# Kernel optimization log

Measured on AMD Instinct MI355X. Metric: run time of the kernel, lower is better.

The kernel has to match this reference:

```python
import jax, jax.numpy as jnp
import numpy as np

V, E, H, L, B, S = 32000, 512, 1024, 2, 128, 256

def setup_inputs() -> dict:
    key = jax.random.key(0)
    ks = jax.random.split(key, 24)
    s = 0.02
    inp = {
        'input_token': jax.random.randint(ks[0], (B, 1), 0, V),
        'hidden': jax.random.normal(ks[1], (L, B, H), jnp.float32),
        'cell': jax.random.normal(ks[2], (L, B, H), jnp.float32),
        'encoder_outputs': jax.random.normal(ks[3], (B, S, H), jnp.float32),
        'embedding': jax.random.normal(ks[4], (V, E), jnp.float32) * s,
        'W1_w': jax.random.normal(ks[5], (H, H), jnp.float32) * s,
        'W1_b': jnp.zeros((H,), jnp.float32),
        'W2_w': jax.random.normal(ks[6], (H, H), jnp.float32) * s,
        'W2_b': jnp.zeros((H,), jnp.float32),
        'V_w': jax.random.normal(ks[7], (1, H), jnp.float32) * s,
        'V_b': jnp.zeros((1,), jnp.float32),
        'w_ih0': jax.random.normal(ks[8], (4 * H, E + H), jnp.float32) * s,
        'w_hh0': jax.random.normal(ks[9], (4 * H, H), jnp.float32) * s,
        'b_ih0': jnp.zeros((4 * H,), jnp.float32),
        'b_hh0': jnp.zeros((4 * H,), jnp.float32),
        'w_ih1': jax.random.normal(ks[10], (4 * H, H), jnp.float32) * s,
        'w_hh1': jax.random.normal(ks[11], (4 * H, H), jnp.float32) * s,
        'b_ih1': jnp.zeros((4 * H,), jnp.float32),
        'b_hh1': jnp.zeros((4 * H,), jnp.float32),
        'fc_w': jax.random.normal(ks[12], (V, 2 * H), jnp.float32) * s,
        'fc_b': jnp.zeros((V,), jnp.float32),
    }
    return inp


def _lstm_cell(x, h, c, w_ih, w_hh, b_ih, b_hh):
    # PyTorch gate order: i, f, g, o
    gates = x @ w_ih.T + b_ih + h @ w_hh.T + b_hh  # [B, 4H]
    i, f, g, o = jnp.split(gates, 4, axis=-1)
    i, f, o = jax.nn.sigmoid(i), jax.nn.sigmoid(f), jax.nn.sigmoid(o)
    g = jnp.tanh(g)
    c_new = f * c + i * g
    h_new = o * jnp.tanh(c_new)
    return h_new, c_new


def reference(input_token, hidden, cell, encoder_outputs, embedding,
              W1_w, W1_b, W2_w, W2_b, V_w, V_b,
              w_ih0, w_hh0, b_ih0, b_hh0, w_ih1, w_hh1, b_ih1, b_hh1,
              fc_w, fc_b):
    emb = embedding[input_token[:, 0]]                       # [B, E]
    h_top = hidden[-1]                                        # [B, H]
    # Bahdanau attention
    energy = jnp.tanh(encoder_outputs @ W1_w.T + W1_b
                      + (h_top @ W2_w.T + W2_b)[:, None, :])  # [B, S, H]
    scores = energy @ V_w.T + V_b                             # [B, S, 1]
    attn = jax.nn.softmax(scores, axis=1)                     # [B, S, 1]
    context = jnp.sum(attn * encoder_outputs, axis=1)         # [B, H]
    # single-step 2-layer LSTM
    x = jnp.concatenate([emb, context], axis=-1)              # [B, E+H]
    h0, c0 = _lstm_cell(x, hidden[0], cell[0], w_ih0, w_hh0, b_ih0, b_hh0)
    h1, c1 = _lstm_cell(h0, hidden[1], cell[1], w_ih1, w_hh1, b_ih1, b_hh1)
    # output projection
    logits = jnp.concatenate([h1, context], axis=-1) @ fc_w.T + fc_b  # [B, V]
    prediction = jax.nn.log_softmax(logits, axis=-1)
    new_hidden = jnp.stack([h0, h1])
    new_cell = jnp.stack([c0, c1])
    return prediction, new_hidden, new_cell, attn
```

## Files before the change

### kernel.cpp

```cpp
#include <hip/hip_runtime.h>

#define H_DIM 1024
#define B_DIM 128
#define S_DIM 256
#define V_DIM 32000
#define E_DIM 512

typedef __bf16 bf16_t;
typedef bf16_t bf16x8 __attribute__((ext_vector_type(8)));
typedef bf16_t bf16x4 __attribute__((ext_vector_type(4)));
typedef float floatx4 __attribute__((ext_vector_type(4)));

#define BM 128
#define BN 128
#define BK 64
#define LDK (BK + 8)

__device__ inline float fast_tanh(float x) {
    x = fminf(fmaxf(x, -15.f), 15.f);
    float e = __expf(2.f * x);
    return (e - 1.f) / (e + 1.f);
}
__device__ inline float sigmoidf_(float x) { return 1.f / (1.f + __expf(-x)); }

__device__ inline bf16x4 cvt4(float4 v) {
    return (bf16x4){(bf16_t)v.x, (bf16_t)v.y, (bf16_t)v.z, (bf16_t)v.w};
}

template <int MODE>
__global__ __launch_bounds__(256) void gemm2(
    const float* __restrict__ A, int lda,
    const float* __restrict__ B1, int ldb1,
    const float* __restrict__ B2, int ldb2, int splitB,
    int K, int kChunk,
    float* __restrict__ C, int ldc,
    const float* __restrict__ bias1, const float* __restrict__ bias2,
    const float* __restrict__ proj, const float* __restrict__ Vw,
    float* __restrict__ scores)
{
    __shared__ bf16_t As[BM][LDK];
    __shared__ bf16_t Bs[BN][LDK];

    const int tid  = threadIdx.x;
    const int wid  = tid >> 6;
    const int lane = tid & 63;
    const int m0 = blockIdx.y * BM;
    const int n0 = blockIdx.x * BN;

    const int wave_m = (wid & 1) * 64;
    const int wave_n = (wid >> 1) * 64;
    const int laneM  = lane & 15;
    const int laneK  = (lane >> 4) * 8;

    const int tk = (tid & 15) * 4;
    const int tr = tid >> 4;

    const int kStart = blockIdx.z * kChunk;
    const int kEnd   = min(K, kStart + kChunk);

    floatx4 acc[4][4];
#pragma unroll
    for (int i = 0; i < 4; i++)
#pragma unroll
        for (int j = 0; j < 4; j++) acc[i][j] = (floatx4)0.f;

    const float* Arow = A + (size_t)(m0 + tr) * lda + tk;

    for (int k0 = kStart; k0 < kEnd; k0 += BK) {
#pragma unroll
        for (int p = 0; p < 8; p++) {
            float4 v = *(const float4*)(Arow + (size_t)(p * 16) * lda + k0);
            *(bf16x4*)(&As[tr + p * 16][tk]) = cvt4(v);
        }
        const float* Bp; size_t ldb; int kb;
        if (k0 < splitB) { Bp = B1; ldb = (size_t)ldb1; kb = k0 + tk; }
        else             { Bp = B2; ldb = (size_t)ldb2; kb = k0 - splitB + tk; }
        const float* Brow = Bp + (size_t)(n0 + tr) * ldb + kb;
#pragma unroll
        for (int p = 0; p < 8; p++) {
            float4 v = *(const float4*)(Brow + (size_t)(p * 16) * ldb);
            *(bf16x4*)(&Bs[tr + p * 16][tk]) = cvt4(v);
        }
        __syncthreads();

#pragma unroll
        for (int kk = 0; kk < 2; kk++) {
            bf16x8 af[4], bfb[4];
#pragma unroll
            for (int mt = 0; mt < 4; mt++)
                af[mt] = *(const bf16x8*)(&As[wave_m + mt * 16 + laneM][kk * 32 + laneK]);
#pragma unroll
            for (int nt = 0; nt < 4; nt++)
                bfb[nt] = *(const bf16x8*)(&Bs[wave_n + nt * 16 + laneM][kk * 32 + laneK]);
#pragma unroll
            for (int mt = 0; mt < 4; mt++)
#pragma unroll
                for (int nt = 0; nt < 4; nt++)
                    acc[mt][nt] = __builtin_amdgcn_mfma_f32_16x16x32_bf16(
                        af[mt], bfb[nt], acc[mt][nt], 0, 0, 0);
        }
        __syncthreads();
    }

    if (MODE == 0 || MODE == 2) {
        const bool addb = (MODE == 0) || (blockIdx.z == 0);
#pragma unroll
        for (int mt = 0; mt < 4; mt++) {
            int mrow = m0 + wave_m + mt * 16 + (lane >> 4) * 4;
#pragma unroll
            for (int nt = 0; nt < 4; nt++) {
                int n = n0 + wave_n + nt * 16 + laneM;
                float bsum = 0.f;
                if (addb) bsum = (bias1 ? bias1[n] : 0.f) + (bias2 ? bias2[n] : 0.f);
#pragma unroll
                for (int r = 0; r < 4; r++) {
                    float val = acc[mt][nt][r] + bsum;
                    if (MODE == 0) C[(size_t)(mrow + r) * ldc + n] = val;
                    else           atomicAdd(&C[(size_t)(mrow + r) * ldc + n], val);
                }
            }
        }
    } else {
#pragma unroll
        for (int mt = 0; mt < 4; mt++) {
#pragma unroll
            for (int r = 0; r < 4; r++) {
                int m = m0 + wave_m + mt * 16 + (lane >> 4) * 4 + r;
                int b = m >> 8;
                float v = 0.f;
#pragma unroll
                for (int nt = 0; nt < 4; nt++) {
                    int n = n0 + wave_n + nt * 16 + laneM;
                    float t = acc[mt][nt][r] + bias1[n] + proj[(size_t)b * H_DIM + n];
                    v += fast_tanh(t) * Vw[n];
                }
#pragma unroll
                for (int off = 1; off < 16; off <<= 1) v += __shfl_xor(v, off, 64);
                if (laneM == 0) atomicAdd(&scores[m], v);
            }
        }
    }
}

__global__ void attn_softmax_kernel(const float* __restrict__ scores,
                                    float* __restrict__ attn_ws,
                                    float* __restrict__ attn_out) {
    __shared__ float red[256];
    int b = blockIdx.x, t = threadIdx.x;
    float v = scores[b * S_DIM + t];
    red[t] = v; __syncthreads();
    for (int off = 128; off > 0; off >>= 1) {
        if (t < off) red[t] = fmaxf(red[t], red[t + off]);
        __syncthreads();
    }
    float mx = red[0]; __syncthreads();
    float e = __expf(v - mx);
    red[t] = e; __syncthreads();
    for (int off = 128; off > 0; off >>= 1) {
        if (t < off) red[t] += red[t + off];
        __syncthreads();
    }
    float a = e / red[0];
    attn_ws[b * S_DIM + t] = a;
    attn_out[b * S_DIM + t] = a;
}

__global__ __launch_bounds__(256) void context_kernel(
    const float* __restrict__ enc, const float* __restrict__ attn,
    float* __restrict__ x0, float* __restrict__ x2) {
    __shared__ float a_s[S_DIM];
    int b = blockIdx.y;
    int h = blockIdx.x * 256 + threadIdx.x;
    a_s[threadIdx.x] = attn[b * S_DIM + threadIdx.x];
    __syncthreads();
    const float* base = enc + (size_t)b * S_DIM * H_DIM + h;
    float acc0 = 0.f, acc1 = 0.f;
#pragma unroll 4
    for (int s = 0; s < S_DIM; s += 2) {
        acc0 += a_s[s]     * base[(size_t)s * H_DIM];
        acc1 += a_s[s + 1] * base[(size_t)(s + 1) * H_DIM];
    }
    float c = acc0 + acc1;
    x0[(size_t)b * 2560 + 512 + h]  = c;
    x2[(size_t)b * 2048 + 1024 + h] = c;
}

__global__ void pack_misc_kernel(const int* __restrict__ tok,
                                 const float* __restrict__ emb_table,
                                 const float* __restrict__ hidden,
                                 float* __restrict__ x0, float* __restrict__ x1) {
    int b = blockIdx.y;
    int k = blockIdx.x * 256 + threadIdx.x;
    if (k < E_DIM)
        x0[(size_t)b * 2560 + k] = emb_table[(size_t)tok[b] * E_DIM + k];
    else if (k < E_DIM + H_DIM)
        x0[(size_t)b * 2560 + 1024 + k] = hidden[b * H_DIM + (k - E_DIM)];
    else
        x1[(size_t)b * 2048 + 1024 + (k - E_DIM - H_DIM)] =
            hidden[(size_t)B_DIM * H_DIM + b * H_DIM + (k - E_DIM - H_DIM)];
}

__global__ void lstm_cell_kernel(const float* __restrict__ gates,
                                 const float* __restrict__ c_in,
                                 float* __restrict__ hx, int hx_stride,
                                 float* __restrict__ h_out,
                                 float* __restrict__ c_out) {
    int b = blockIdx.y;
    int n = blockIdx.x * 256 + threadIdx.x;
    const float* g = gates + (size_t)b * 4 * H_DIM;
    float i  = sigmoidf_(g[n]);
    float f  = sigmoidf_(g[H_DIM + n]);
    float gg = fast_tanh(g[2 * H_DIM + n]);
    float o  = sigmoidf_(g[3 * H_DIM + n]);
    float c  = f * c_in[b * H_DIM + n] + i * gg;
    float h  = o * fast_tanh(c);
    hx[(size_t)b * hx_stride + n] = h;
    h_out[b * H_DIM + n] = h;
    c_out[b * H_DIM + n] = c;
}

__global__ __launch_bounds__(1024) void log_softmax_kernel(float* logits) {
    __shared__ float red[1024];
    int b = blockIdx.x, t = threadIdx.x;
    float* row = logits + (size_t)b * V_DIM;
    float mx = -1e30f;
    for (int v = t; v < V_DIM; v += 1024) mx = fmaxf(mx, row[v]);
    red[t] = mx; __syncthreads();
    for (int off = 512; off > 0; off >>= 1) {
        if (t < off) red[t] = fmaxf(red[t], red[t + off]);
        __syncthreads();
    }
    mx = red[0]; __syncthreads();
    float s = 0.f;
    for (int v = t; v < V_DIM; v += 1024) s += __expf(row[v] - mx);
    red[t] = s; __syncthreads();
    for (int off = 512; off > 0; off >>= 1) {
        if (t < off) red[t] += red[t + off];
        __syncthreads();
    }
    float lse = mx + __logf(red[0]);
    for (int v = t; v < V_DIM; v += 1024) row[v] = row[v] - lse;
}

extern "C" void kernel_launch(void* const* d_in, const int* in_sizes, int n_in,
                              void* d_out, int out_size, void* d_ws, size_t ws_size,
                              hipStream_t stream) {
    const int*   tok    = (const int*)  d_in[0];
    const float* hidden = (const float*)d_in[1];
    const float* cell   = (const float*)d_in[2];
    const float* enc    = (const float*)d_in[3];
    const float* embt   = (const float*)d_in[4];
    const float* W1w    = (const float*)d_in[5];
    const float* W1b    = (const float*)d_in[6];
    const float* W2w    = (const float*)d_in[7];
    const float* W2b    = (const float*)d_in[8];
    const float* Vw     = (const float*)d_in[9];
    const float* wih0 = (const float*)d_in[11];
    const float* whh0 = (const float*)d_in[12];
    const float* bih0 = (const float*)d_in[13];
    const float* bhh0 = (const float*)d_in[14];
    const float* wih1 = (const float*)d_in[15];
    const float* whh1 = (const float*)d_in[16];
    const float* bih1 = (const float*)d_in[17];
    const float* bhh1 = (const float*)d_in[18];
    const float* fcw  = (const float*)d_in[19];
    const float* fcb  = (const float*)d_in[20];

    float* out        = (float*)d_out;
    float* pred       = out;
    float* out_hidden = out + (size_t)B_DIM * V_DIM;
    float* out_cell   = out_hidden + 2 * B_DIM * H_DIM;
    float* out_attn   = out_cell + 2 * B_DIM * H_DIM;

    float* ws     = (float*)d_ws;
    float* scores = ws;
    float* proj   = scores + 32768;
    float* gatesA = proj + 131072;
    float* gatesB = gatesA + 524288;
    float* attnw  = gatesB + 524288;
    float* x0     = attnw + 32768;
    float* x1     = x0 + 327680;
    float* x2     = x1 + 262144;

    hipMemsetAsync(ws, 0, (size_t)(32768 + 131072 + 2 * 524288) * sizeof(float), stream);

    dim3 blk(256);
    pack_misc_kernel<<<dim3(10, B_DIM), blk, 0, stream>>>(tok, embt, hidden, x0, x1);

    gemm2<2><<<dim3(8, 1, 2), blk, 0, stream>>>(
        hidden + (size_t)B_DIM * H_DIM, H_DIM, W2w, H_DIM, nullptr, 0, H_DIM,
        H_DIM, 512, proj, H_DIM, W2b, nullptr, nullptr, nullptr, nullptr);

    gemm2<1><<<dim3(8, 256, 1), blk, 0, stream>>>(
        enc, H_DIM, W1w, H_DIM, nullptr, 0, H_DIM,
        H_DIM, H_DIM, nullptr, 0, W1b, nullptr, proj, Vw, scores);

    attn_softmax_kernel<<<B_DIM, 256, 0, stream>>>(scores, attnw, out_attn);
    context_kernel<<<dim3(4, B_DIM), blk, 0, stream>>>(enc, attnw, x0, x2);

    gemm2<2><<<dim3(32, 1, 4), blk, 0, stream>>>(
        x0, 2560, wih0, 1536, whh0, H_DIM, 1536,
        2560, 640, gatesA, 4096, bih0, bhh0, nullptr, nullptr, nullptr);
    lstm_cell_kernel<<<dim3(4, B_DIM), blk, 0, stream>>>(
        gatesA, cell, x1, 2048, out_hidden, out_cell);

    gemm2<2><<<dim3(32, 1, 4), blk, 0, stream>>>(
        x1, 2048, wih1, H_DIM, whh1, H_DIM, H_DIM,
        2048, 512, gatesB, 4096, bih1, bhh1, nullptr, nullptr, nullptr);
    lstm_cell_kernel<<<dim3(4, B_DIM), blk, 0, stream>>>(
        gatesB, cell + (size_t)B_DIM * H_DIM, x2, 2048,
        out_hidden + (size_t)B_DIM * H_DIM, out_cell + (size_t)B_DIM * H_DIM);

    gemm2<0><<<dim3(250, 1, 1), blk, 0, stream>>>(
        x2, 2048, fcw, 2048, nullptr, 0, 2048,
        2048, 2048, pred, V_DIM, fcb, nullptr, nullptr, nullptr, nullptr);

    log_softmax_kernel<<<B_DIM, 1024, 0, stream>>>(pred);
}
```

Baseline: 813.1 us.

## Overhaul decoder kernels: bf16 scores GEMM, prefetch, split-K partials, fused softmax-context

Adds register prefetch of the next K tile in the generic GEMM, fuses attention softmax with the context reduction, and replaces atomic split-K with separate partial buffers that the LSTM cell and log-softmax kernels sum. When the workspace is large enough, it converts encoder outputs and W1 to bf16 and runs a dedicated scores GEMM that loads straight into LDS with a swizzled layout. The FC projection is split over K to raise occupancy. The cost is extra conversion passes over the 32 MB encoder tensor on every call, more workspace traffic for the partials, and paths chosen by workspace size.

```diff
diff --git a/kernel.cpp b/kernel.cpp
--- a/kernel.cpp
+++ b/kernel.cpp
@@ -22,9 +22,103 @@
     return (e - 1.f) / (e + 1.f);
 }
 __device__ inline float sigmoidf_(float x) { return 1.f / (1.f + __expf(-x)); }
-
 __device__ inline bf16x4 cvt4(float4 v) {
     return (bf16x4){(bf16_t)v.x, (bf16_t)v.y, (bf16_t)v.z, (bf16_t)v.w};
+}
+__device__ __forceinline__ void gload16(const bf16_t* g, bf16_t* l) {
+    __builtin_amdgcn_global_load_lds(
+        (const __attribute__((address_space(1))) void*)g,
+        (__attribute__((address_space(3))) void*)l, 16, 0, 0);
+}
+
+__global__ __launch_bounds__(256) void gemm_scores_bf16(
+    const bf16_t* __restrict__ A, const bf16_t* __restrict__ B,
+    const float* __restrict__ bias1, const float* __restrict__ proj,
+    const float* __restrict__ Vw, float* __restrict__ scores)
+{
+    __shared__ bf16_t As[128 * 64];
+    __shared__ bf16_t Bs[128 * 64];
+
+    const int tid  = threadIdx.x;
+    const int wid  = tid >> 6;
+    const int lane = tid & 63;
+    const int m0 = blockIdx.y * BM;
+    const int n0 = blockIdx.x * BN;
+
+    const int wave_m = (wid & 1) * 64;
+    const int wave_n = (wid >> 1) * 64;
+    const int laneM  = lane & 15;
+    const int laneG  = lane >> 4;
+
+    const int srow = lane >> 3;
+    const int pc   = lane & 7;
+
+    floatx4 acc[4][4];
+#pragma unroll
+    for (int i = 0; i < 4; i++)
+#pragma unroll
+        for (int j = 0; j < 4; j++) acc[i][j] = (floatx4)0.f;
+
+    for (int k0 = 0; k0 < H_DIM; k0 += BK) {
+#pragma unroll
+        for (int i = 0; i < 4; i++) {
+            int r  = wid * 32 + i * 8 + srow;
+            int lc = pc ^ (r & 7);
+            gload16(A + (size_t)(m0 + r) * H_DIM + k0 + lc * 8,
+                    As + (wid * 32 + i * 8) * 64);
+        }
+#pragma unroll
+        for (int i = 0; i < 4; i++) {
+            int r  = wid * 32 + i * 8 + srow;
+            int lc = pc ^ (r & 7);
+            gload16(B + (size_t)(n0 + r) * H_DIM + k0 + lc * 8,
+                    Bs + (wid * 32 + i * 8) * 64);
+        }
+        __syncthreads();
+
+#pragma unroll
+        for (int kk = 0; kk < 2; kk++) {
+            bf16x8 af[4], bfb[4];
+#pragma unroll
+            for (int mt = 0; mt < 4; mt++) {
+                int ra = wave_m + mt * 16 + laneM;
+                int pa = (kk * 4 + laneG) ^ (ra & 7);
+                af[mt] = *(const bf16x8*)(&As[ra * 64 + pa * 8]);
+            }
+#pragma unroll
+            for (int nt = 0; nt < 4; nt++) {
+                int rb = wave_n + nt * 16 + laneM;
+                int pb = (kk * 4 + laneG) ^ (rb & 7);
+                bfb[nt] = *(const bf16x8*)(&Bs[rb * 64 + pb * 8]);
+            }
+#pragma unroll
+            for (int mt = 0; mt < 4; mt++)
+#pragma unroll
+                for (int nt = 0; nt < 4; nt++)
+                    acc[mt][nt] = __builtin_amdgcn_mfma_f32_16x16x32_bf16(
+                        af[mt], bfb[nt], acc[mt][nt], 0, 0, 0);
+        }
+        __syncthreads();
+    }
+
+#pragma unroll
+    for (int mt = 0; mt < 4; mt++) {
+#pragma unroll
+        for (int r = 0; r < 4; r++) {
+            int m = m0 + wave_m + mt * 16 + (lane >> 4) * 4 + r;
+            int b = m >> 8;
+            float v = 0.f;
+#pragma unroll
+            for (int nt = 0; nt < 4; nt++) {
+                int n = n0 + wave_n + nt * 16 + laneM;
+                float t = acc[mt][nt][r] + bias1[n] + proj[(size_t)b * H_DIM + n];
+                v += fast_tanh(t) * Vw[n];
+            }
+#pragma unroll
+            for (int off = 1; off < 16; off <<= 1) v += __shfl_xor(v, off, 64);
+            if (laneM == 0) atomicAdd(&scores[m], v);
+        }
+    }
 }
 
 template <int MODE>
@@ -34,6 +128,7 @@
     const float* __restrict__ B2, int ldb2, int splitB,
     int K, int kChunk,
     float* __restrict__ C, int ldc,
+    float* __restrict__ Cpart, long long partStride,
     const float* __restrict__ bias1, const float* __restrict__ bias2,
     const float* __restrict__ proj, const float* __restrict__ Vw,
     float* __restrict__ scores)
@@ -66,23 +161,31 @@
 
     const float* Arow = A + (size_t)(m0 + tr) * lda + tk;
 
-    for (int k0 = kStart; k0 < kEnd; k0 += BK) {
-#pragma unroll
-        for (int p = 0; p < 8; p++) {
-            float4 v = *(const float4*)(Arow + (size_t)(p * 16) * lda + k0);
-            *(bf16x4*)(&As[tr + p * 16][tk]) = cvt4(v);
-        }
+    float4 ar[8], br[8];
+    auto loadA = [&](int k0) {
+#pragma unroll
+        for (int p = 0; p < 8; p++)
+            ar[p] = *(const float4*)(Arow + (size_t)(p * 16) * lda + k0);
+    };
+    auto loadB = [&](int k0) {
         const float* Bp; size_t ldb; int kb;
         if (k0 < splitB) { Bp = B1; ldb = (size_t)ldb1; kb = k0 + tk; }
         else             { Bp = B2; ldb = (size_t)ldb2; kb = k0 - splitB + tk; }
         const float* Brow = Bp + (size_t)(n0 + tr) * ldb + kb;
 #pragma unroll
-        for (int p = 0; p < 8; p++) {
-            float4 v = *(const float4*)(Brow + (size_t)(p * 16) * ldb);
-            *(bf16x4*)(&Bs[tr + p * 16][tk]) = cvt4(v);
-        }
-        __syncthreads();
-
+        for (int p = 0; p < 8; p++)
+            br[p] = *(const float4*)(Brow + (size_t)(p * 16) * ldb);
+    };
+
+    loadA(kStart); loadB(kStart);
+
+    for (int k0 = kStart; k0 < kEnd; k0 += BK) {
+#pragma unroll
+        for (int p = 0; p < 8; p++) *(bf16x4*)(&As[tr + p * 16][tk]) = cvt4(ar[p]);
+#pragma unroll
+        for (int p = 0; p < 8; p++) *(bf16x4*)(&Bs[tr + p * 16][tk]) = cvt4(br[p]);
+        __syncthreads();
+        if (k0 + BK < kEnd) { loadA(k0 + BK); loadB(k0 + BK); }
 #pragma unroll
         for (int kk = 0; kk < 2; kk++) {
             bf16x8 af[4], bfb[4];
@@ -102,8 +205,11 @@
         __syncthreads();
     }
 
-    if (MODE == 0 || MODE == 2) {
-        const bool addb = (MODE == 0) || (blockIdx.z == 0);
+    if (MODE == 2 || MODE == 3) {
+        const bool addb = (blockIdx.z == 0);
+        float* dst = C;
+        if (MODE == 3 && blockIdx.z > 0)
+            dst = Cpart + (size_t)(blockIdx.z - 1) * partStride;
 #pragma unroll
         for (int mt = 0; mt < 4; mt++) {
             int mrow = m0 + wave_m + mt * 16 + (lane >> 4) * 4;
@@ -115,8 +221,8 @@
 #pragma unroll
                 for (int r = 0; r < 4; r++) {
                     float val = acc[mt][nt][r] + bsum;
-                    if (MODE == 0) C[(size_t)(mrow + r) * ldc + n] = val;
-                    else           atomicAdd(&C[(size_t)(mrow + r) * ldc + n], val);
+                    if (MODE == 2) atomicAdd(&C[(size_t)(mrow + r) * ldc + n], val);
+                    else           dst[(size_t)(mrow + r) * ldc + n] = val;
                 }
             }
         }
@@ -142,10 +248,23 @@
     }
 }
 
-__global__ void attn_softmax_kernel(const float* __restrict__ scores,
-                                    float* __restrict__ attn_ws,
-                                    float* __restrict__ attn_out) {
+__global__ void convert_kernel(const float* __restrict__ src,
+                               bf16_t* __restrict__ dst, int n4) {
+    int i = blockIdx.x * blockDim.x + threadIdx.x;
+    int stride = gridDim.x * blockDim.x;
+    for (; i < n4; i += stride) {
+        float4 v = ((const float4*)src)[i];
+        ((bf16x4*)dst)[i] = cvt4(v);
+    }
+}
+
+template <typename T>
+__global__ __launch_bounds__(256) void softmax_context_kernel(
+    const T* __restrict__ enc, const float* __restrict__ scores,
+    float* __restrict__ out_attn, float* __restrict__ x0, float* __restrict__ x2)
+{
     __shared__ float red[256];
+    __shared__ float a_s[256];
     int b = blockIdx.x, t = threadIdx.x;
     float v = scores[b * S_DIM + t];
     red[t] = v; __syncthreads();
@@ -161,28 +280,29 @@
         __syncthreads();
     }
     float a = e / red[0];
-    attn_ws[b * S_DIM + t] = a;
-    attn_out[b * S_DIM + t] = a;
-}
-
-__global__ __launch_bounds__(256) void context_kernel(
-    const float* __restrict__ enc, const float* __restrict__ attn,
-    float* __restrict__ x0, float* __restrict__ x2) {
-    __shared__ float a_s[S_DIM];
-    int b = blockIdx.y;
-    int h = blockIdx.x * 256 + threadIdx.x;
-    a_s[threadIdx.x] = attn[b * S_DIM + threadIdx.x];
+    out_attn[b * S_DIM + t] = a;
+    a_s[t] = a;
     __syncthreads();
-    const float* base = enc + (size_t)b * S_DIM * H_DIM + h;
-    float acc0 = 0.f, acc1 = 0.f;
+
+    const T* base = enc + (size_t)b * S_DIM * H_DIM;
+    float c0 = 0.f, c1 = 0.f, c2 = 0.f, c3 = 0.f;
 #pragma unroll 4
-    for (int s = 0; s < S_DIM; s += 2) {
-        acc0 += a_s[s]     * base[(size_t)s * H_DIM];
-        acc1 += a_s[s + 1] * base[(size_t)(s + 1) * H_DIM];
-    }
-    float c = acc0 + acc1;
-    x0[(size_t)b * 2560 + 512 + h]  = c;
-    x2[(size_t)b * 2048 + 1024 + h] = c;
+    for (int s = 0; s < S_DIM; s++) {
+        float aw = a_s[s];
+        const T* row = base + (size_t)s * H_DIM + t;
+        c0 += aw * (float)row[0];
+        c1 += aw * (float)row[256];
+        c2 += aw * (float)row[512];
+        c3 += aw * (float)row[768];
+    }
+    x0[(size_t)b * 2560 + 512 + t]        = c0;
+    x0[(size_t)b * 2560 + 512 + t + 256]  = c1;
+    x0[(size_t)b * 2560 + 512 + t + 512]  = c2;
+    x0[(size_t)b * 2560 + 512 + t + 768]  = c3;
+    x2[(size_t)b * 2048 + 1024 + t]       = c0;
+    x2[(size_t)b * 2048 + 1024 + t + 256] = c1;
+    x2[(size_t)b * 2048 + 1024 + t + 512] = c2;
+    x2[(size_t)b * 2048 + 1024 + t + 768] = c3;
 }
 
 __global__ void pack_misc_kernel(const int* __restrict__ tok,
@@ -201,30 +321,52 @@
 }
 
 __global__ void lstm_cell_kernel(const float* __restrict__ gates,
+                                 const float* __restrict__ gpart, int nExtra,
+                                 long long partStride,
                                  const float* __restrict__ c_in,
                                  float* __restrict__ hx, int hx_stride,
                                  float* __restrict__ h_out,
                                  float* __restrict__ c_out) {
     int b = blockIdx.y;
     int n = blockIdx.x * 256 + threadIdx.x;
-    const float* g = gates + (size_t)b * 4 * H_DIM;
-    float i  = sigmoidf_(g[n]);
-    float f  = sigmoidf_(g[H_DIM + n]);
-    float gg = fast_tanh(g[2 * H_DIM + n]);
-    float o  = sigmoidf_(g[3 * H_DIM + n]);
-    float c  = f * c_in[b * H_DIM + n] + i * gg;
-    float h  = o * fast_tanh(c);
+    size_t base = (size_t)b * 4 * H_DIM;
+    float gi = gates[base + n];
+    float gf = gates[base + H_DIM + n];
+    float gg = gates[base + 2 * H_DIM + n];
+    float go = gates[base + 3 * H_DIM + n];
+    for (int p = 0; p < nExtra; p++) {
+        size_t pb = (size_t)p * partStride + base;
+        gi += gpart[pb + n];
+        gf += gpart[pb + H_DIM + n];
+        gg += gpart[pb + 2 * H_DIM + n];
+        go += gpart[pb + 3 * H_DIM + n];
+    }
+    float i = sigmoidf_(gi), f = sigmoidf_(gf), o = sigmoidf_(go);
+    float g = fast_tanh(gg);
+    float c = f * c_in[b * H_DIM + n] + i * g;
+    float h = o * fast_tanh(c);
     hx[(size_t)b * hx_stride + n] = h;
     h_out[b * H_DIM + n] = h;
     c_out[b * H_DIM + n] = c;
 }
 
-__global__ __launch_bounds__(1024) void log_softmax_kernel(float* logits) {
+__global__ __launch_bounds__(1024) void log_softmax_kernel(
+    float* __restrict__ pred, const float* __restrict__ part) {
     __shared__ float red[1024];
     int b = blockIdx.x, t = threadIdx.x;
-    float* row = logits + (size_t)b * V_DIM;
+    float lv[32];
     float mx = -1e30f;
-    for (int v = t; v < V_DIM; v += 1024) mx = fmaxf(mx, row[v]);
+#pragma unroll
+    for (int j = 0; j < 32; j++) {
+        int v = t + j * 1024;
+        float x = -1e30f;
+        if (v < V_DIM) {
+            x = pred[(size_t)b * V_DIM + v];
+            if (part) x += part[(size_t)b * V_DIM + v];
+        }
+        lv[j] = x;
+        mx = fmaxf(mx, x);
+    }
     red[t] = mx; __syncthreads();
     for (int off = 512; off > 0; off >>= 1) {
         if (t < off) red[t] = fmaxf(red[t], red[t + off]);
@@ -232,14 +374,19 @@
     }
     mx = red[0]; __syncthreads();
     float s = 0.f;
-    for (int v = t; v < V_DIM; v += 1024) s += __expf(row[v] - mx);
+#pragma unroll
+    for (int j = 0; j < 32; j++) s += __expf(lv[j] - mx);
     red[t] = s; __syncthreads();
     for (int off = 512; off > 0; off >>= 1) {
         if (t < off) red[t] += red[t + off];
         __syncthreads();
     }
     float lse = mx + __logf(red[0]);
-    for (int v = t; v < V_DIM; v += 1024) row[v] = row[v] - lse;
+#pragma unroll
+    for (int j = 0; j < 32; j++) {
+        int v = t + j * 1024;
+        if (v < V_DIM) pred[(size_t)b * V_DIM + v] = lv[j] - lse;
+    }
 }
 
 extern "C" void kernel_launch(void* const* d_in, const int* in_sizes, int n_in,
@@ -272,48 +419,91 @@
     float* out_cell   = out_hidden + 2 * B_DIM * H_DIM;
     float* out_attn   = out_cell + 2 * B_DIM * H_DIM;
 
-    float* ws     = (float*)d_ws;
-    float* scores = ws;
-    float* proj   = scores + 32768;
-    float* gatesA = proj + 131072;
-    float* gatesB = gatesA + 524288;
-    float* attnw  = gatesB + 524288;
-    float* x0     = attnw + 32768;
-    float* x1     = x0 + 327680;
-    float* x2     = x1 + 262144;
-
-    hipMemsetAsync(ws, 0, (size_t)(32768 + 131072 + 2 * 524288) * sizeof(float), stream);
+    float* ws      = (float*)d_ws;
+    float* scores  = ws;
+    float* proj    = ws + 32768;
+    float* gatesA  = ws + 163840;
+    float* gatesB  = ws + 688128;
+    float* x0      = ws + 1212416;
+    float* x1      = ws + 1540096;
+    float* x2      = ws + 1802240;
+    float* gAp     = ws + 2064384;
+    float* gBp     = ws + 3637248;
+    float* fcpart  = ws + 5210112;
+    bf16_t* encbf  = (bf16_t*)(ws + 9306112);
+    bf16_t* W1bf   = (bf16_t*)(ws + 26083328);
+
+    const bool pathA = ws_size >= (size_t)26607616 * 4;
+    const bool pathB = !pathA && ws_size >= (size_t)9306112 * 4 + 16384000;
+    const bool split = pathA || pathB;
 
     dim3 blk(256);
+
+    if (split)
+        hipMemsetAsync(ws, 0, (size_t)163840 * 4, stream);
+    else
+        hipMemsetAsync(ws, 0, (size_t)1212416 * 4, stream);
+
     pack_misc_kernel<<<dim3(10, B_DIM), blk, 0, stream>>>(tok, embt, hidden, x0, x1);
 
     gemm2<2><<<dim3(8, 1, 2), blk, 0, stream>>>(
         hidden + (size_t)B_DIM * H_DIM, H_DIM, W2w, H_DIM, nullptr, 0, H_DIM,
-        H_DIM, 512, proj, H_DIM, W2b, nullptr, nullptr, nullptr, nullptr);
-
-    gemm2<1><<<dim3(8, 256, 1), blk, 0, stream>>>(
-        enc, H_DIM, W1w, H_DIM, nullptr, 0, H_DIM,
-        H_DIM, H_DIM, nullptr, 0, W1b, nullptr, proj, Vw, scores);
-
-    attn_softmax_kernel<<<B_DIM, 256, 0, stream>>>(scores, attnw, out_attn);
-    context_kernel<<<dim3(4, B_DIM), blk, 0, stream>>>(enc, attnw, x0, x2);
-
-    gemm2<2><<<dim3(32, 1, 4), blk, 0, stream>>>(
-        x0, 2560, wih0, 1536, whh0, H_DIM, 1536,
-        2560, 640, gatesA, 4096, bih0, bhh0, nullptr, nullptr, nullptr);
-    lstm_cell_kernel<<<dim3(4, B_DIM), blk, 0, stream>>>(
-        gatesA, cell, x1, 2048, out_hidden, out_cell);
-
-    gemm2<2><<<dim3(32, 1, 4), blk, 0, stream>>>(
-        x1, 2048, wih1, H_DIM, whh1, H_DIM, H_DIM,
-        2048, 512, gatesB, 4096, bih1, bhh1, nullptr, nullptr, nullptr);
-    lstm_cell_kernel<<<dim3(4, B_DIM), blk, 0, stream>>>(
-        gatesB, cell + (size_t)B_DIM * H_DIM, x2, 2048,
-        out_hidden + (size_t)B_DIM * H_DIM, out_cell + (size_t)B_DIM * H_DIM);
-
-    gemm2<0><<<dim3(250, 1, 1), blk, 0, stream>>>(
-        x2, 2048, fcw, 2048, nullptr, 0, 2048,
-        2048, 2048, pred, V_DIM, fcb, nullptr, nullptr, nullptr, nullptr);
-
-    log_softmax_kernel<<<B_DIM, 1024, 0, stream>>>(pred);
-}
+        H_DIM, 512, proj, H_DIM, nullptr, 0, W2b, nullptr, nullptr, nullptr, nullptr);
+
+    if (pathA) {
+        convert_kernel<<<4096, blk, 0, stream>>>(enc, encbf, 8388608);
+        convert_kernel<<<1024, blk, 0, stream>>>(W1w, W1bf, 262144);
+        gemm_scores_bf16<<<dim3(8, 256), blk, 0, stream>>>(
+            encbf, W1bf, W1b, proj, Vw, scores);
+        softmax_context_kernel<bf16_t><<<B_DIM, 256, 0, stream>>>(
+            encbf, scores, out_attn, x0, x2);
+    } else {
+        gemm2<1><<<dim3(8, 256, 1), blk, 0, stream>>>(
+            enc, H_DIM, W1w, H_DIM, nullptr, 0, H_DIM,
+            H_DIM, H_DIM, nullptr, 0, nullptr, 0, W1b, nullptr, proj, Vw, scores);
+        softmax_context_kernel<float><<<B_DIM, 256, 0, stream>>>(
+            enc, scores, out_attn, x0, x2);
+    }
+
+    if (split) {
+        gemm2<3><<<dim3(32, 1, 4), blk, 0, stream>>>(
+            x0, 2560, wih0, 1536, whh0, H_DIM, 1536, 2560, 640,
+            gatesA, 4096, gAp, 524288, bih0, bhh0, nullptr, nullptr, nullptr);
+        lstm_cell_kernel<<<dim3(4, B_DIM), blk, 0, stream>>>(
+            gatesA, gAp, 3, 524288, cell, x1, 2048, out_hidden, out_cell);
+    } else {
+        gemm2<2><<<dim3(32, 1, 4), blk, 0, stream>>>(
+            x0, 2560, wih0, 1536, whh0, H_DIM, 1536, 2560, 640,
+            gatesA, 4096, nullptr, 0, bih0, bhh0, nullptr, nullptr, nullptr);
+        lstm_cell_kernel<<<dim3(4, B_DIM), blk, 0, stream>>>(
+            gatesA, nullptr, 0, 0, cell, x1, 2048, out_hidden, out_cell);
+    }
+
+    if (split) {
+        gemm2<3><<<dim3(32, 1, 4), blk, 0, stream>>>(
+            x1, 2048, wih1, H_DIM, whh1, H_DIM, H_DIM, 2048, 512,
+            gatesB, 4096, gBp, 524288, bih1, bhh1, nullptr, nullptr, nullptr);
+        lstm_cell_kernel<<<dim3(4, B_DIM), blk, 0, stream>>>(
+            gatesB, gBp, 3, 524288, cell + (size_t)B_DIM * H_DIM, x2, 2048,
+            out_hidden + (size_t)B_DIM * H_DIM, out_cell + (size_t)B_DIM * H_DIM);
+    } else {
+        gemm2<2><<<dim3(32, 1, 4), blk, 0, stream>>>(
+            x1, 2048, wih1, H_DIM, whh1, H_DIM, H_DIM, 2048, 512,
+            gatesB, 4096, nullptr, 0, bih1, bhh1, nullptr, nullptr, nullptr);
+        lstm_cell_kernel<<<dim3(4, B_DIM), blk, 0, stream>>>(
+            gatesB, nullptr, 0, 0, cell + (size_t)B_DIM * H_DIM, x2, 2048,
+            out_hidden + (size_t)B_DIM * H_DIM, out_cell + (size_t)B_DIM * H_DIM);
+    }
+
+    if (split) {
+        gemm2<3><<<dim3(250, 1, 2), blk, 0, stream>>>(
+            x2, 2048, fcw, 2048, nullptr, 0, 2048, 2048, 1024,
+            pred, V_DIM, fcpart, 4096000, fcb, nullptr, nullptr, nullptr, nullptr);
+        log_softmax_kernel<<<B_DIM, 1024, 0, stream>>>(pred, fcpart);
+    } else {
+        gemm2<3><<<dim3(250, 1, 1), blk, 0, stream>>>(
+            x2, 2048, fcw, 2048, nullptr, 0, 2048, 2048, 2048,
+            pred, V_DIM, nullptr, 0, fcb, nullptr, nullptr, nullptr, nullptr);
+        log_softmax_kernel<<<B_DIM, 1024, 0, stream>>>(pred, nullptr);
+    }
+}
```

Result: faster. 776.1 us (-4.6%).
